# Performance work log

Hardware: AMD Instinct MI355X
Metric: run time of the kernel (lower is better)

Reference implementation:

```python
import jax, jax.numpy as jnp
import numpy as np


def _xavier(key, shape):
    fan_out, fan_in = shape[0], shape[1]
    lim = np.sqrt(6.0 / (fan_in + fan_out)).astype(np.float32)
    return jax.random.uniform(key, shape, jnp.float32, -lim, lim)


def setup_inputs() -> dict:
    key = jax.random.key(0)
    ks = jax.random.split(key, 28)
    B, D, G, ND = 16384, 32, 6, 8
    V_user, V_item, V_gender, V_age, V_occ, V_genre = 1000000, 100000, 2, 7, 21, 19
    H1, H2 = 128, 64
    deep_in = 6 * D + ND  # 200
    return {
        "user_id": jax.random.randint(ks[0], (B,), 0, V_user),
        "item_id": jax.random.randint(ks[1], (B,), 0, V_item),
        "user_gender": jax.random.randint(ks[2], (B,), 0, V_gender),
        "user_age": jax.random.randint(ks[3], (B,), 0, V_age),
        "user_occupation": jax.random.randint(ks[4], (B,), 0, V_occ),
        "item_genre_ids": jax.random.randint(ks[5], (B, G), 0, V_genre),
        "item_genre_mask": jax.random.randint(ks[6], (B, G), 0, 2).astype(jnp.float32),
        "dense_features": jax.random.normal(ks[7], (B, ND), jnp.float32),
        # first-order (1-dim) embedding tables
        "fo_user": _xavier(ks[8], (V_user, 1)),
        "fo_item": _xavier(ks[9], (V_item, 1)),
        "fo_gender": _xavier(ks[10], (V_gender, 1)),
        "fo_age": _xavier(ks[11], (V_age, 1)),
        "fo_occ": _xavier(ks[12], (V_occ, 1)),
        "fo_genre": _xavier(ks[13], (V_genre, 1)),
        # second-order / deep embedding tables
        "emb_user": _xavier(ks[14], (V_user, D)),
        "emb_item": _xavier(ks[15], (V_item, D)),
        "emb_gender": _xavier(ks[16], (V_gender, D)),
        "emb_age": _xavier(ks[17], (V_age, D)),
        "emb_occ": _xavier(ks[18], (V_occ, D)),
        "emb_genre": _xavier(ks[19], (V_genre, D)),
        # dense linear + deep MLP
        "dense_W": _xavier(ks[20], (1, ND)),
        "dense_b": jnp.zeros((1,), jnp.float32),
        "W1": _xavier(ks[21], (H1, deep_in)),
        "b1": jnp.zeros((H1,), jnp.float32),
        "W2": _xavier(ks[22], (H2, H1)),
        "b2": jnp.zeros((H2,), jnp.float32),
        "Wout": _xavier(ks[23], (1, H2)),
        "bout": jnp.zeros((1,), jnp.float32),
    }


def _pool(table, ids, mask):
    # masked mean-pool over the genre list axis
    e = table[ids]                       # [B, G, d]
    m = mask[..., None]                  # [B, G, 1]
    denom = jnp.clip(m.sum(axis=1), 1.0)  # [B, 1]
    return (e * m).sum(axis=1) / denom   # [B, d]


def reference(user_id, item_id, user_gender, user_age, user_occupation,
              item_genre_ids, item_genre_mask, dense_features,
              fo_user, fo_item, fo_gender, fo_age, fo_occ, fo_genre,
              emb_user, emb_item, emb_gender, emb_age, emb_occ, emb_genre,
              dense_W, dense_b, W1, b1, W2, b2, Wout, bout):
    # FM first order: sum of 1-dim gathers + pooled genre + dense linear -> [B,1]
    first = (fo_user[user_id] + fo_item[item_id] + fo_gender[user_gender]
             + fo_age[user_age] + fo_occ[user_occupation]
             + _pool(fo_genre, item_genre_ids, item_genre_mask)
             + dense_features @ dense_W.T + dense_b)
    # FM second order: stack field embeddings [B, 6, D]
    x = jnp.stack([emb_user[user_id], emb_item[item_id], emb_gender[user_gender],
                   emb_age[user_age], emb_occ[user_occupation],
                   _pool(emb_genre, item_genre_ids, item_genre_mask)], axis=1)
    s = x.sum(axis=1)                                   # [B, D]
    second = 0.5 * (s * s - (x * x).sum(axis=1)).sum(axis=1, keepdims=True)  # [B,1]
    # deep part (dropout is identity in eval mode)
    deep_in = jnp.concatenate([x.reshape(x.shape[0], -1), dense_features], axis=1)
    h = jax.nn.relu(deep_in @ W1.T + b1)
    h = jax.nn.relu(h @ W2.T + b2)
    deep = h @ Wout.T + bout                            # [B,1]
    return (first + second + deep).squeeze(1)           # [B]
```

## Files before the change

### kernel.cpp

```cpp
#include <hip/hip_runtime.h>


typedef float v2f __attribute__((ext_vector_type(2)));
static __device__ __forceinline__ v2f bc2(float x) { v2f r; r.x = x; r.y = x; return r; }
static __device__ __forceinline__ float relu1(float x) { return fmaxf(x, 0.f); }

#define ROWS_PER_BLOCK 16
#define ROWS_PER_WAVE 4
#define DI_STRIDE 204
#define H1_STRIDE 132

__global__ void pack_weights(const float* __restrict__ W1, const float* __restrict__ W2,
                             float4* __restrict__ W1p, float4* __restrict__ W2p) {
    const int idx = blockIdx.x * blockDim.x + threadIdx.x;
    if (idx < 6400) {
        const int s = idx & 1, jp = (idx >> 1) & 15, k4 = (idx >> 5) % 50, w = idx / 1600;
        const int j0 = w * 32 + 2 * jp, c = 4 * k4 + 2 * s;
        W1p[idx] = make_float4(W1[j0 * 200 + c],     W1[(j0 + 1) * 200 + c],
                               W1[j0 * 200 + c + 1], W1[(j0 + 1) * 200 + c + 1]);
    }
    if (idx < 2048) {
        const int s = idx & 1, jp = (idx >> 1) & 7, k4 = (idx >> 4) & 31, w = idx >> 9;
        const int j0 = w * 16 + 2 * jp, c = 4 * k4 + 2 * s;
        W2p[idx] = make_float4(W2[j0 * 128 + c],     W2[(j0 + 1) * 128 + c],
                               W2[j0 * 128 + c + 1], W2[(j0 + 1) * 128 + c + 1]);
    }
}

__global__ __launch_bounds__(256) void deepfm_kernel(
    const int* __restrict__ user_id, const int* __restrict__ item_id,
    const int* __restrict__ gender_, const int* __restrict__ age_,
    const int* __restrict__ occ_, const int* __restrict__ genre_ids,
    const float* __restrict__ genre_mask, const float* __restrict__ dense,
    const float* __restrict__ fo_user, const float* __restrict__ fo_item,
    const float* __restrict__ fo_gender, const float* __restrict__ fo_age,
    const float* __restrict__ fo_occ, const float* __restrict__ fo_genre,
    const float* __restrict__ emb_user, const float* __restrict__ emb_item,
    const float* __restrict__ emb_gender, const float* __restrict__ emb_age,
    const float* __restrict__ emb_occ, const float* __restrict__ emb_genre,
    const float* __restrict__ dense_W, const float* __restrict__ dense_b,
    const float4* __restrict__ W1p, const float* __restrict__ b1,
    const float4* __restrict__ W2p, const float* __restrict__ b2,
    const float* __restrict__ Wout, const float* __restrict__ bout,
    float* __restrict__ out, int B)
{
    __shared__ float lds_di[ROWS_PER_BLOCK][DI_STRIDE];
    __shared__ float lds_rs[ROWS_PER_BLOCK];
    __shared__ float lds_part[ROWS_PER_BLOCK][4];

    const int tid = threadIdx.x;
    const int wid = tid >> 6;
    const int lane = tid & 63;
    const int blockRow0 = blockIdx.x * ROWS_PER_BLOCK;

    {
        const int rowBase = blockRow0 + wid * ROWS_PER_WAVE;

        #pragma unroll 1
        for (int r = 0; r < ROWS_PER_WAVE; ++r) {
            int row = rowBase + r; if (row >= B) row = B - 1;
            const int ri = wid * ROWS_PER_WAVE + r;

            const int uid = user_id[row], iid = item_id[row];
            const int gg = gender_[row], aa = age_[row], oo = occ_[row];

            int gid[6]; float mk[6]; float msum = 0.f;
            #pragma unroll
            for (int t = 0; t < 6; ++t) {
                gid[t] = genre_ids[row * 6 + t];
                mk[t]  = genre_mask[row * 6 + t];
                msum  += mk[t];
            }
            const float inv_den = 1.0f / fmaxf(msum, 1.0f);

            float pe_sum = 0.f, pe_sq = 0.f;
            {
                float v = (lane < 32) ? emb_user[(size_t)uid * 32 + lane]
                                      : emb_item[(size_t)iid * 32 + (lane - 32)];
                lds_di[ri][lane] = v;
                pe_sum += v; pe_sq += v * v;
            }
            {
                float v = (lane < 32) ? emb_gender[gg * 32 + lane]
                                      : emb_age[aa * 32 + (lane - 32)];
                lds_di[ri][64 + lane] = v;
                pe_sum += v; pe_sq += v * v;
            }
            {
                float v;
                if (lane < 32) {
                    v = emb_occ[oo * 32 + lane];
                } else {
                    const int d = lane - 32;
                    float s = 0.f;
                    #pragma unroll
                    for (int t = 0; t < 6; ++t) s += mk[t] * emb_genre[gid[t] * 32 + d];
                    v = s * inv_den;
                }
                lds_di[ri][128 + lane] = v;
                pe_sum += v; pe_sq += v * v;
            }
            if (lane < 8) lds_di[ri][192 + lane] = dense[(size_t)row * 8 + lane];

            float s2 = pe_sum + __shfl_xor(pe_sum, 32);
            float ss = pe_sq  + __shfl_xor(pe_sq, 32);
            float t2 = 0.5f * (s2 * s2 - ss);
            #pragma unroll
            for (int off = 16; off >= 1; off >>= 1) t2 += __shfl_xor(t2, off);

            float fo = fo_user[uid] + fo_item[iid] + fo_gender[gg]
                     + fo_age[aa] + fo_occ[oo];
            float fg = 0.f;
            #pragma unroll
            for (int t = 0; t < 6; ++t) fg += mk[t] * fo_genre[gid[t]];
            fo += fg * inv_den;
            float dd = 0.f;
            #pragma unroll
            for (int j = 0; j < 8; ++j) dd += dense[(size_t)row * 8 + j] * dense_W[j];
            fo += dd + dense_b[0];

            if (lane == 0) lds_rs[ri] = fo + t2;
        }
    }
    __syncthreads();

    const int jp1 = lane & 15;
    const int rh  = lane >> 4;

    v2f acc[ROWS_PER_WAVE];
    #pragma unroll
    for (int r = 0; r < ROWS_PER_WAVE; ++r) acc[r] = bc2(0.f);

    {
        const float4* __restrict__ W1b = W1p + wid * 1600;
        const float4* __restrict__ dv = reinterpret_cast<const float4*>(&lds_di[0][0]);

        #pragma unroll 2
        for (int k4 = 0; k4 < 50; ++k4) {
            const float4 wa = W1b[(k4 * 16 + jp1) * 2 + 0];
            const float4 wb = W1b[(k4 * 16 + jp1) * 2 + 1];
            const v2f w0 = { wa.x, wa.y }, w1 = { wa.z, wa.w };
            const v2f w2 = { wb.x, wb.y }, w3 = { wb.z, wb.w };
            #pragma unroll
            for (int r = 0; r < ROWS_PER_WAVE; ++r) {
                const float4 a = dv[(rh + 4 * r) * 51 + k4];
                acc[r] = __builtin_elementwise_fma(w0, bc2(a.x), acc[r]);
                acc[r] = __builtin_elementwise_fma(w1, bc2(a.y), acc[r]);
                acc[r] = __builtin_elementwise_fma(w2, bc2(a.z), acc[r]);
                acc[r] = __builtin_elementwise_fma(w3, bc2(a.w), acc[r]);
            }
        }
    }
    __syncthreads();

    float* __restrict__ h1b = &lds_di[0][0];
    {
        const int j0 = wid * 32 + 2 * jp1;
        const float2 bb = *reinterpret_cast<const float2*>(b1 + j0);
        #pragma unroll
        for (int r = 0; r < ROWS_PER_WAVE; ++r) {
            const int row = rh + 4 * r;
            reinterpret_cast<float2*>(h1b)[(row * H1_STRIDE + j0) >> 1] =
                make_float2(relu1(acc[r].x + bb.x), relu1(acc[r].y + bb.y));
        }
    }
    __syncthreads();

    const int jp2 = lane & 7;
    const int rh2 = lane >> 3;

    v2f acc2[2];
    acc2[0] = bc2(0.f); acc2[1] = bc2(0.f);

    {
        const float4* __restrict__ W2b = W2p + wid * 512;
        const float4* __restrict__ h1v = reinterpret_cast<const float4*>(h1b);

        #pragma unroll 2
        for (int k4 = 0; k4 < 32; ++k4) {
            const float4 wa = W2b[(k4 * 8 + jp2) * 2 + 0];
            const float4 wb = W2b[(k4 * 8 + jp2) * 2 + 1];
            const v2f w0 = { wa.x, wa.y }, w1 = { wa.z, wa.w };
            const v2f w2 = { wb.x, wb.y }, w3 = { wb.z, wb.w };
            #pragma unroll
            for (int t = 0; t < 2; ++t) {
                const float4 h = h1v[(rh2 + 8 * t) * 33 + k4];
                acc2[t] = __builtin_elementwise_fma(w0, bc2(h.x), acc2[t]);
                acc2[t] = __builtin_elementwise_fma(w1, bc2(h.y), acc2[t]);
                acc2[t] = __builtin_elementwise_fma(w2, bc2(h.z), acc2[t]);
                acc2[t] = __builtin_elementwise_fma(w3, bc2(h.w), acc2[t]);
            }
        }
    }

    {
        const int j0 = wid * 16 + 2 * jp2;
        const float2 bb2 = *reinterpret_cast<const float2*>(b2 + j0);
        const float2 wo  = *reinterpret_cast<const float2*>(Wout + j0);
        #pragma unroll
        for (int t = 0; t < 2; ++t) {
            const float h2x = relu1(acc2[t].x + bb2.x);
            const float h2y = relu1(acc2[t].y + bb2.y);
            float v = wo.x * h2x + wo.y * h2y;
            v += __shfl_xor(v, 1); v += __shfl_xor(v, 2); v += __shfl_xor(v, 4);
            if (jp2 == 0) lds_part[rh2 + 8 * t][wid] = v;
        }
    }
    __syncthreads();

    if (tid < ROWS_PER_BLOCK) {
        const int row = blockRow0 + tid;
        if (row < B) {
            const float deep = lds_part[tid][0] + lds_part[tid][1]
                             + lds_part[tid][2] + lds_part[tid][3] + bout[0];
            out[row] = deep + lds_rs[tid];
        }
    }
}

extern "C" void kernel_launch(void* const* d_in, const int* in_sizes, int n_in,
                              void* d_out, int out_size, void* d_ws, size_t ws_size,
                              hipStream_t stream) {
    const int B = in_sizes[0];

    float4* W1p = reinterpret_cast<float4*>(d_ws);
    float4* W2p = reinterpret_cast<float4*>((char*)d_ws + 102400);

    pack_weights<<<25, 256, 0, stream>>>(
        (const float*)d_in[22], (const float*)d_in[24], W1p, W2p);

    const int grid = (B + ROWS_PER_BLOCK - 1) / ROWS_PER_BLOCK;
    deepfm_kernel<<<grid, 256, 0, stream>>>(
        (const int*)d_in[0],  (const int*)d_in[1],  (const int*)d_in[2],
        (const int*)d_in[3],  (const int*)d_in[4],  (const int*)d_in[5],
        (const float*)d_in[6],  (const float*)d_in[7],
        (const float*)d_in[8],  (const float*)d_in[9],  (const float*)d_in[10],
        (const float*)d_in[11], (const float*)d_in[12], (const float*)d_in[13],
        (const float*)d_in[14], (const float*)d_in[15], (const float*)d_in[16],
        (const float*)d_in[17], (const float*)d_in[18], (const float*)d_in[19],
        (const float*)d_in[20], (const float*)d_in[21],
        W1p, (const float*)d_in[23],
        W2p, (const float*)d_in[25],
        (const float*)d_in[26], (const float*)d_in[27],
        (float*)d_out, B);
}
```

Measured before the change: 255.2 us.

## Gather all four wave rows at once with float2 lanes instead of a serial row loop

```diff
diff --git a/kernel.cpp b/kernel.cpp
--- a/kernel.cpp
+++ b/kernel.cpp
@@ -54,73 +54,71 @@
     const int blockRow0 = blockIdx.x * ROWS_PER_BLOCK;
 
     {
-        const int rowBase = blockRow0 + wid * ROWS_PER_WAVE;
-
-        #pragma unroll 1
-        for (int r = 0; r < ROWS_PER_WAVE; ++r) {
-            int row = rowBase + r; if (row >= B) row = B - 1;
-            const int ri = wid * ROWS_PER_WAVE + r;
-
-            const int uid = user_id[row], iid = item_id[row];
-            const int gg = gender_[row], aa = age_[row], oo = occ_[row];
-
-            int gid[6]; float mk[6]; float msum = 0.f;
-            #pragma unroll
-            for (int t = 0; t < 6; ++t) {
-                gid[t] = genre_ids[row * 6 + t];
-                mk[t]  = genre_mask[row * 6 + t];
-                msum  += mk[t];
-            }
-            const float inv_den = 1.0f / fmaxf(msum, 1.0f);
-
-            float pe_sum = 0.f, pe_sq = 0.f;
-            {
-                float v = (lane < 32) ? emb_user[(size_t)uid * 32 + lane]
-                                      : emb_item[(size_t)iid * 32 + (lane - 32)];
-                lds_di[ri][lane] = v;
-                pe_sum += v; pe_sq += v * v;
-            }
-            {
-                float v = (lane < 32) ? emb_gender[gg * 32 + lane]
-                                      : emb_age[aa * 32 + (lane - 32)];
-                lds_di[ri][64 + lane] = v;
-                pe_sum += v; pe_sq += v * v;
-            }
-            {
-                float v;
-                if (lane < 32) {
-                    v = emb_occ[oo * 32 + lane];
-                } else {
-                    const int d = lane - 32;
-                    float s = 0.f;
-                    #pragma unroll
-                    for (int t = 0; t < 6; ++t) s += mk[t] * emb_genre[gid[t] * 32 + d];
-                    v = s * inv_den;
-                }
-                lds_di[ri][128 + lane] = v;
-                pe_sum += v; pe_sq += v * v;
-            }
-            if (lane < 8) lds_di[ri][192 + lane] = dense[(size_t)row * 8 + lane];
-
-            float s2 = pe_sum + __shfl_xor(pe_sum, 32);
-            float ss = pe_sq  + __shfl_xor(pe_sq, 32);
-            float t2 = 0.5f * (s2 * s2 - ss);
-            #pragma unroll
-            for (int off = 16; off >= 1; off >>= 1) t2 += __shfl_xor(t2, off);
-
-            float fo = fo_user[uid] + fo_item[iid] + fo_gender[gg]
-                     + fo_age[aa] + fo_occ[oo];
+        const int rl = lane & 3;
+        const int dx = lane >> 2;
+        const int d0 = 2 * dx;
+
+        int row = blockRow0 + wid * ROWS_PER_WAVE + rl;
+        if (row >= B) row = B - 1;
+        const int ri = wid * ROWS_PER_WAVE + rl;
+
+        const int uid = user_id[row], iid = item_id[row];
+        const int gg = gender_[row], aa = age_[row], oo = occ_[row];
+
+        int gid[6]; float mk[6]; float msum = 0.f;
+        #pragma unroll
+        for (int t = 0; t < 6; ++t) {
+            gid[t] = genre_ids[row * 6 + t];
+            mk[t]  = genre_mask[row * 6 + t];
+            msum  += mk[t];
+        }
+        const float inv_den = 1.0f / fmaxf(msum, 1.0f);
+
+        const float2 eu = *reinterpret_cast<const float2*>(emb_user + (size_t)uid * 32 + d0);
+        const float2 ei = *reinterpret_cast<const float2*>(emb_item + (size_t)iid * 32 + d0);
+        const float2 eg = *reinterpret_cast<const float2*>(emb_gender + gg * 32 + d0);
+        const float2 ea = *reinterpret_cast<const float2*>(emb_age + aa * 32 + d0);
+        const float2 eo = *reinterpret_cast<const float2*>(emb_occ + oo * 32 + d0);
+        float epx = 0.f, epy = 0.f;
+        #pragma unroll
+        for (int t = 0; t < 6; ++t) {
+            const float2 g = *reinterpret_cast<const float2*>(emb_genre + gid[t] * 32 + d0);
+            epx += mk[t] * g.x; epy += mk[t] * g.y;
+        }
+        epx *= inv_den; epy *= inv_den;
+
+        *reinterpret_cast<float2*>(&lds_di[ri][d0])       = eu;
+        *reinterpret_cast<float2*>(&lds_di[ri][32 + d0])  = ei;
+        *reinterpret_cast<float2*>(&lds_di[ri][64 + d0])  = eg;
+        *reinterpret_cast<float2*>(&lds_di[ri][96 + d0])  = ea;
+        *reinterpret_cast<float2*>(&lds_di[ri][128 + d0]) = eo;
+        *reinterpret_cast<float2*>(&lds_di[ri][160 + d0]) = make_float2(epx, epy);
+
+        const float sx = eu.x + ei.x + eg.x + ea.x + eo.x + epx;
+        const float sy = eu.y + ei.y + eg.y + ea.y + eo.y + epy;
+        const float qx = eu.x*eu.x + ei.x*ei.x + eg.x*eg.x + ea.x*ea.x + eo.x*eo.x + epx*epx;
+        const float qy = eu.y*eu.y + ei.y*ei.y + eg.y*eg.y + ea.y*ea.y + eo.y*eo.y + epy*epy;
+        float c = 0.5f * ((sx * sx - qx) + (sy * sy - qy));
+
+        if (dx < 4) {
+            const float2 dv = *reinterpret_cast<const float2*>(dense + (size_t)row * 8 + d0);
+            *reinterpret_cast<float2*>(&lds_di[ri][192 + d0]) = dv;
+            c += dv.x * dense_W[d0] + dv.y * dense_W[d0 + 1];
+        } else if (dx == 8)  c += fo_user[uid];
+        else if (dx == 9)  c += fo_item[iid];
+        else if (dx == 10) c += fo_gender[gg];
+        else if (dx == 11) c += fo_age[aa];
+        else if (dx == 12) c += fo_occ[oo];
+        else if (dx == 13) {
             float fg = 0.f;
             #pragma unroll
             for (int t = 0; t < 6; ++t) fg += mk[t] * fo_genre[gid[t]];
-            fo += fg * inv_den;
-            float dd = 0.f;
-            #pragma unroll
-            for (int j = 0; j < 8; ++j) dd += dense[(size_t)row * 8 + j] * dense_W[j];
-            fo += dd + dense_b[0];
-
-            if (lane == 0) lds_rs[ri] = fo + t2;
-        }
+            c += fg * inv_den;
+        } else if (dx == 14) c += dense_b[0];
+
+        c += __shfl_xor(c, 4); c += __shfl_xor(c, 8);
+        c += __shfl_xor(c, 16); c += __shfl_xor(c, 32);
+        if (dx == 0) lds_rs[ri] = c;
     }
     __syncthreads();
 
```

Result: faster. 248.2 us (-2.7%).
